# Performance work log

Hardware: AMD Instinct MI355X
Metric: run time of the kernel (lower is better)

Reference implementation:

```python
import jax, jax.numpy as jnp
import numpy as np

B, N, CIN, D, H = 4, 8192, 64, 64, 8  # batch, grid points, in_ch, per-head dim, heads
EPS = 1e-5


def layernorm(x, w, b):
    # x: [b, h, l, d]; w, b: [h, d] (per-head affine), normalize over last dim
    mu = jnp.mean(x, axis=-1, keepdims=True)
    var = jnp.var(x, axis=-1, keepdims=True)
    xn = (x - mu) * jax.lax.rsqrt(var + EPS)
    return xn * w[None, :, None, :] + b[None, :, None, :]


def setup_inputs() -> dict:
    key = jax.random.key(0)
    ks = jax.random.split(key, 12)
    hd = H * D
    s_in = 1.0 / np.sqrt(CIN)
    s_hd = 1.0 / np.sqrt(hd)
    return {
        "v": jax.random.normal(ks[0], (B, N, CIN), jnp.float32),
        "Wq_w": jax.random.uniform(ks[1], (hd, CIN), jnp.float32, -s_in, s_in),
        "Wq_b": jax.random.uniform(ks[2], (hd,), jnp.float32, -s_in, s_in),
        "Wk_w": jax.random.uniform(ks[3], (hd, CIN), jnp.float32, -s_in, s_in),
        "Wk_b": jax.random.uniform(ks[4], (hd,), jnp.float32, -s_in, s_in),
        "Wv_w": jax.random.uniform(ks[5], (hd, CIN), jnp.float32, -s_in, s_in),
        "Wv_b": jax.random.uniform(ks[6], (hd,), jnp.float32, -s_in, s_in),
        "lnq_w": jnp.ones((H, D), jnp.float32),
        "lnq_b": jnp.zeros((H, D), jnp.float32),
        "lnk_w": jnp.ones((H, D), jnp.float32),
        "lnk_b": jnp.zeros((H, D), jnp.float32),
        "o_w": jax.random.uniform(ks[7], (D, hd), jnp.float32, -s_hd, s_hd),
        "o_b": jax.random.uniform(ks[8], (D,), jnp.float32, -s_hd, s_hd),
    }


def reference(v, Wq_w, Wq_b, Wk_w, Wk_b, Wv_w, Wv_b,
              lnq_w, lnq_b, lnk_w, lnk_b, o_w, o_b):
    b, n, _ = v.shape
    # projections: [b, l, h*d] -> [b, h, l, d]
    def proj(w, bias):
        x = v @ w.T + bias
        return x.reshape(b, n, H, D).transpose(0, 2, 1, 3)
    Q = layernorm(proj(Wq_w, Wq_b), lnq_w, lnq_b)
    K = layernorm(proj(Wk_w, Wk_b), lnk_w, lnk_b)
    V = proj(Wv_w, Wv_b)
    # (Q K^T) V == Q (K^T V): no softmax, so reassociate to O(n d^2)
    KV = jnp.einsum('bhnd,bhne->bhde', K, V)      # [b, h, d, d]
    out = jnp.einsum('bhmd,bhde->bhme', Q, KV)    # [b, h, n, d]
    out = out.transpose(0, 2, 1, 3).reshape(b, n, H * D)
    out = out @ o_w.T + o_b
    return out / n
```

## Files before the change

### kernel.cpp

```cpp
#include <hip/hip_runtime.h>
#include <hip/hip_bf16.h>

#define B_   4
#define N_   8192
#define CIN_ 64
#define H_   8
#define HD_  512
#define EPS_ 1e-5f

typedef __bf16 bf16x8 __attribute__((ext_vector_type(8)));
typedef __bf16 bf16x4 __attribute__((ext_vector_type(4)));
typedef float  f32x4  __attribute__((ext_vector_type(4)));

constexpr size_t OFF_V    = 0;
constexpr size_t SZ_V     = (size_t)B_ * N_ * CIN_ * 2;
constexpr size_t OFF_WQ   = OFF_V + SZ_V;
constexpr size_t SZ_W     = (size_t)HD_ * CIN_ * 2;
constexpr size_t OFF_WK   = OFF_WQ + SZ_W;
constexpr size_t OFF_WV   = OFF_WK + SZ_W;
constexpr size_t OFF_MT   = OFF_WV + SZ_W;
constexpr size_t SZ_MT    = (size_t)B_ * 64 * HD_ * 2;
constexpr size_t OFF_PART = OFF_MT + SZ_MT;
constexpr size_t SZ_PART  = (size_t)B_ * H_ * 16 * 64 * 64 * 4;
constexpr size_t WS_NEED  = OFF_PART + SZ_PART;

template <int CTRL>
__device__ __forceinline__ float dpp_radd(float x) {
  union { float f; int i; } u, v;
  u.f = x;
  v.i = __builtin_amdgcn_update_dpp(0, u.i, CTRL, 0xF, 0xF, false);
  return x + v.f;
}
__device__ __forceinline__ float red16(float x) {
  x = dpp_radd<0x121>(x);
  x = dpp_radd<0x122>(x);
  x = dpp_radd<0x124>(x);
  x = dpp_radd<0x128>(x);
  return x;
}

__global__ __launch_bounds__(256) void prep_cast(
    const float* __restrict__ v, const float* __restrict__ wq,
    const float* __restrict__ wk, const float* __restrict__ wv,
    __bf16* __restrict__ vb, __bf16* __restrict__ wqb,
    __bf16* __restrict__ wkb, __bf16* __restrict__ wvb) {
  const int NV4 = B_ * N_ * CIN_ / 4;
  const int NW4 = HD_ * CIN_ / 4;
  int i = blockIdx.x * 256 + threadIdx.x;
  const float* src; __bf16* dst; int j;
  if (i < NV4)                { src = v;  dst = vb;  j = i; }
  else if (i < NV4 + NW4)     { src = wq; dst = wqb; j = i - NV4; }
  else if (i < NV4 + 2 * NW4) { src = wk; dst = wkb; j = i - NV4 - NW4; }
  else                        { src = wv; dst = wvb; j = i - NV4 - 2 * NW4; }
  const float4 f = reinterpret_cast<const float4*>(src)[j];
  bf16x4 o;
  o[0] = (__bf16)f.x; o[1] = (__bf16)f.y; o[2] = (__bf16)f.z; o[3] = (__bf16)f.w;
  reinterpret_cast<bf16x4*>(dst)[j] = o;
}

__global__ __launch_bounds__(256, 2) void k1_kv(
    const __bf16* __restrict__ vb, const __bf16* __restrict__ wkb,
    const __bf16* __restrict__ wvb, const float* __restrict__ kbias,
    const float* __restrict__ vbias, const float* __restrict__ lnkw,
    const float* __restrict__ lnkb, float* __restrict__ part) {
  const int ch = blockIdx.x, h = blockIdx.y, b = blockIdx.z;
  const int tid = threadIdx.x, w = tid >> 6, lane = tid & 63;
  const int l15 = lane & 15, g = lane >> 4;
  __shared__ alignas(16) char smem[73728];
  __bf16 (*Kt)[72] = reinterpret_cast<__bf16(*)[72]>(smem + w * 18432);
  __bf16 (*Vt)[72] = reinterpret_cast<__bf16(*)[72]>(smem + w * 18432 + 9216);

  const f32x4 z4 = {0.f, 0.f, 0.f, 0.f};
  f32x4 kv[4][4];
#pragma unroll
  for (int i = 0; i < 4; ++i)
#pragma unroll
    for (int j = 0; j < 4; ++j) kv[i][j] = z4;

  float kb[4], vbi[4], lw[4], lb[4];
#pragma unroll
  for (int c = 0; c < 4; ++c) {
    const int col = h * 64 + c * 16 + l15;
    kb[c] = kbias[col]; vbi[c] = vbias[col];
    lw[c] = lnkw[col];  lb[c] = lnkb[col];
  }
  bf16x8 wkf[4][2], wvf[4][2];
#pragma unroll
  for (int c = 0; c < 4; ++c)
#pragma unroll
    for (int kk = 0; kk < 2; ++kk) {
      wkf[c][kk] = *reinterpret_cast<const bf16x8*>(
          wkb + (size_t)(h * 64 + c * 16 + l15) * CIN_ + kk * 32 + g * 8);
      wvf[c][kk] = *reinterpret_cast<const bf16x8*>(
          wvb + (size_t)(h * 64 + c * 16 + l15) * CIN_ + kk * 32 + g * 8);
    }

  for (int t = 0; t < 2; ++t) {
    const int row0 = ch * 512 + w * 128 + t * 64;
    bf16x8 av[4][2];
#pragma unroll
    for (int m = 0; m < 4; ++m)
#pragma unroll
      for (int kk = 0; kk < 2; ++kk)
        av[m][kk] = *reinterpret_cast<const bf16x8*>(
            vb + ((size_t)b * N_ + row0 + m * 16 + l15) * CIN_ + kk * 32 + g * 8);

#pragma unroll
    for (int mp = 0; mp < 2; ++mp) {
      f32x4 acc[2][4];
#pragma unroll
      for (int mi = 0; mi < 2; ++mi)
#pragma unroll
        for (int c = 0; c < 4; ++c) {
          f32x4 a = z4;
          a = __builtin_amdgcn_mfma_f32_16x16x32_bf16(av[mp * 2 + mi][0], wkf[c][0], a, 0, 0, 0);
          a = __builtin_amdgcn_mfma_f32_16x16x32_bf16(av[mp * 2 + mi][1], wkf[c][1], a, 0, 0, 0);
          acc[mi][c] = a;
        }
#pragma unroll
      for (int mi = 0; mi < 2; ++mi) {
        const int m = mp * 2 + mi;
        float s[4] = {0, 0, 0, 0}, ss[4] = {0, 0, 0, 0};
#pragma unroll
        for (int c = 0; c < 4; ++c)
#pragma unroll
          for (int r = 0; r < 4; ++r) {
            float x = acc[mi][c][r] + kb[c];
            acc[mi][c][r] = x;
            s[r] += x; ss[r] += x * x;
          }
#pragma unroll
        for (int r = 0; r < 4; ++r) {
          const float S = red16(s[r]), Q = red16(ss[r]);
          const float mu = S * (1.f / 64.f);
          const float var = Q * (1.f / 64.f) - mu * mu;
          const float rstd = rsqrtf(var + EPS_);
#pragma unroll
          for (int c = 0; c < 4; ++c)
            acc[mi][c][r] = (acc[mi][c][r] - mu) * rstd * lw[c] + lb[c];
        }
#pragma unroll
        for (int c = 0; c < 4; ++c) {
          bf16x4 p;
#pragma unroll
          for (int r = 0; r < 4; ++r) p[r] = (__bf16)acc[mi][c][r];
          *reinterpret_cast<bf16x4*>(&Kt[c * 16 + l15][m * 16 + g * 4]) = p;
        }
      }
    }
#pragma unroll
    for (int mp = 0; mp < 2; ++mp) {
      f32x4 acc[2][4];
#pragma unroll
      for (int mi = 0; mi < 2; ++mi)
#pragma unroll
        for (int c = 0; c < 4; ++c) {
          f32x4 a = z4;
          a = __builtin_amdgcn_mfma_f32_16x16x32_bf16(av[mp * 2 + mi][0], wvf[c][0], a, 0, 0, 0);
          a = __builtin_amdgcn_mfma_f32_16x16x32_bf16(av[mp * 2 + mi][1], wvf[c][1], a, 0, 0, 0);
          acc[mi][c] = a;
        }
#pragma unroll
      for (int mi = 0; mi < 2; ++mi) {
        const int m = mp * 2 + mi;
#pragma unroll
        for (int c = 0; c < 4; ++c) {
          bf16x4 p;
#pragma unroll
          for (int r = 0; r < 4; ++r) p[r] = (__bf16)(acc[mi][c][r] + vbi[c]);
          *reinterpret_cast<bf16x4*>(&Vt[c * 16 + l15][m * 16 + g * 4]) = p;
        }
      }
    }

    __syncthreads();

    bf16x8 va[4][2];
#pragma unroll
    for (int et = 0; et < 4; ++et)
#pragma unroll
      for (int nk = 0; nk < 2; ++nk)
        va[et][nk] = *reinterpret_cast<const bf16x8*>(&Vt[et * 16 + l15][nk * 32 + g * 8]);
#pragma unroll
    for (int dt = 0; dt < 4; ++dt) {
      bf16x8 ka[2];
#pragma unroll
      for (int nk = 0; nk < 2; ++nk)
        ka[nk] = *reinterpret_cast<const bf16x8*>(&Kt[dt * 16 + l15][nk * 32 + g * 8]);
#pragma unroll
      for (int et = 0; et < 4; ++et) {
        kv[dt][et] = __builtin_amdgcn_mfma_f32_16x16x32_bf16(ka[0], va[et][0], kv[dt][et], 0, 0, 0);
        kv[dt][et] = __builtin_amdgcn_mfma_f32_16x16x32_bf16(ka[1], va[et][1], kv[dt][et], 0, 0, 0);
      }
    }

    __syncthreads();
  }

  float* red = reinterpret_cast<float*>(smem + w * 17408);
#pragma unroll
  for (int dt = 0; dt < 4; ++dt)
#pragma unroll
    for (int et = 0; et < 4; ++et)
      *reinterpret_cast<f32x4*>(red + (et * 16 + l15) * 68 + dt * 16 + g * 4) = kv[dt][et];
  __syncthreads();
  float* p0 = part + (size_t)((b * H_ + h) * 16 + ch) * 4096;
#pragma unroll
  for (int k = 0; k < 4; ++k) {
    const int idx4 = tid + k * 256;
    const int e = idx4 >> 4, d = (idx4 & 15) * 4;
    f32x4 sum = *reinterpret_cast<const f32x4*>(
        reinterpret_cast<const float*>(smem) + e * 68 + d);
#pragma unroll
    for (int ww = 1; ww < 4; ++ww)
      sum += *reinterpret_cast<const f32x4*>(
          reinterpret_cast<const float*>(smem + ww * 17408) + e * 68 + d);
    *reinterpret_cast<f32x4*>(p0 + idx4 * 4) = sum;
  }
}

__global__ __launch_bounds__(256) void k2_mt(const float* __restrict__ part,
                                             const float* __restrict__ ow,
                                             __bf16* __restrict__ Mt) {
  const int h = blockIdx.x, b = blockIdx.y;
  const int tid = threadIdx.x;
  __shared__ float KVt[64][64];
  __shared__ float OWl[64][64];
  const float* p0 = part + (size_t)((b * H_ + h) * 16) * 4096;
  for (int i = tid; i < 4096; i += 256) {
    float s = 0.f;
#pragma unroll
    for (int c = 0; c < 16; ++c) s += p0[(size_t)c * 4096 + i];
    (&KVt[0][0])[i] = s;
  }
  for (int i = tid; i < 4096; i += 256) {
    int E = i >> 6, c = i & 63;
    OWl[E][c] = ow[(size_t)E * HD_ + h * 64 + c];
  }
  __syncthreads();
  for (int i = tid; i < 4096; i += 256) {
    int E = i >> 6, d = i & 63;
    float s = 0.f;
#pragma unroll
    for (int c = 0; c < 64; ++c) s += KVt[c][d] * OWl[E][c];
    Mt[(size_t)(b * 64 + E) * HD_ + h * 64 + d] = (__bf16)(s * (1.0f / N_));
  }
}

__global__ __launch_bounds__(256, 2) void k3_out(
    const __bf16* __restrict__ vb, const __bf16* __restrict__ wqb,
    const float* __restrict__ qbias, const float* __restrict__ lnqw,
    const float* __restrict__ lnqb, const __bf16* __restrict__ Mt,
    const float* __restrict__ obias, float* __restrict__ out) {
  const int nt = blockIdx.x, b = blockIdx.y;
  const int tid = threadIdx.x, w = tid >> 6, lane = tid & 63;
  const int l15 = lane & 15, g = lane >> 4;
  __shared__ __bf16 Qt[64][520];
  const int row0 = nt * 64;
  const f32x4 z4 = {0.f, 0.f, 0.f, 0.f};

  bf16x8 bv[4][2];
#pragma unroll
  for (int c = 0; c < 4; ++c)
#pragma unroll
    for (int kk = 0; kk < 2; ++kk)
      bv[c][kk] = *reinterpret_cast<const bf16x8*>(
          vb + ((size_t)b * N_ + row0 + c * 16 + l15) * CIN_ + kk * 32 + g * 8);

#pragma unroll
  for (int hh = 0; hh < 2; ++hh) {
    const int h = w * 2 + hh;
    bf16x8 aw[4][2];
#pragma unroll
    for (int mj = 0; mj < 4; ++mj)
#pragma unroll
      for (int kk = 0; kk < 2; ++kk)
        aw[mj][kk] = *reinterpret_cast<const bf16x8*>(
            wqb + (size_t)(h * 64 + mj * 16 + l15) * CIN_ + kk * 32 + g * 8);
    f32x4 qb4[4], lw4[4], lb4[4];
#pragma unroll
    for (int mj = 0; mj < 4; ++mj) {
      const int base = h * 64 + mj * 16 + g * 4;
      qb4[mj] = *reinterpret_cast<const f32x4*>(qbias + base);
      lw4[mj] = *reinterpret_cast<const f32x4*>(lnqw + base);
      lb4[mj] = *reinterpret_cast<const f32x4*>(lnqb + base);
    }
    f32x4 acc[4][4];
#pragma unroll
    for (int mj = 0; mj < 4; ++mj)
#pragma unroll
      for (int c = 0; c < 4; ++c) {
        f32x4 a = z4;
        a = __builtin_amdgcn_mfma_f32_16x16x32_bf16(aw[mj][0], bv[c][0], a, 0, 0, 0);
        a = __builtin_amdgcn_mfma_f32_16x16x32_bf16(aw[mj][1], bv[c][1], a, 0, 0, 0);
        acc[mj][c] = a;
      }
#pragma unroll
    for (int c = 0; c < 4; ++c) {
      float s = 0.f, ss = 0.f;
#pragma unroll
      for (int mj = 0; mj < 4; ++mj)
#pragma unroll
        for (int r = 0; r < 4; ++r) {
          float x = acc[mj][c][r] + qb4[mj][r];
          acc[mj][c][r] = x;
          s += x; ss += x * x;
        }
      s += __shfl_xor(s, 16); ss += __shfl_xor(ss, 16);
      s += __shfl_xor(s, 32); ss += __shfl_xor(ss, 32);
      const float mu = s * (1.f / 64.f);
      const float var = ss * (1.f / 64.f) - mu * mu;
      const float rstd = rsqrtf(var + EPS_);
#pragma unroll
      for (int mj = 0; mj < 4; ++mj)
#pragma unroll
        for (int r = 0; r < 4; ++r)
          acc[mj][c][r] = (acc[mj][c][r] - mu) * rstd * lw4[mj][r] + lb4[mj][r];
    }
#pragma unroll
    for (int mj = 0; mj < 4; ++mj)
#pragma unroll
      for (int c = 0; c < 4; ++c) {
        bf16x4 p;
#pragma unroll
        for (int r = 0; r < 4; ++r) p[r] = (__bf16)acc[mj][c][r];
        *reinterpret_cast<bf16x4*>(&Qt[c * 16 + l15][h * 64 + mj * 16 + g * 4]) = p;
      }
  }
  __syncthreads();

  f32x4 acc2[4];
#pragma unroll
  for (int et = 0; et < 4; ++et) acc2[et] = z4;
  for (int kk = 0; kk < 16; ++kk) {
    bf16x8 aq = *reinterpret_cast<const bf16x8*>(&Qt[w * 16 + l15][kk * 32 + g * 8]);
#pragma unroll
    for (int et = 0; et < 4; ++et) {
      bf16x8 bm = *reinterpret_cast<const bf16x8*>(
          Mt + (size_t)(b * 64 + et * 16 + l15) * HD_ + kk * 32 + g * 8);
      acc2[et] = __builtin_amdgcn_mfma_f32_16x16x32_bf16(aq, bm, acc2[et], 0, 0, 0);
    }
  }
#pragma unroll
  for (int et = 0; et < 4; ++et) {
    const float ob = obias[et * 16 + l15] * (1.0f / N_);
#pragma unroll
    for (int r = 0; r < 4; ++r)
      out[((size_t)b * N_ + row0 + w * 16 + g * 4 + r) * 64 + et * 16 + l15] =
          acc2[et][r] + ob;
  }
}

extern "C" void kernel_launch(void* const* d_in, const int* in_sizes, int n_in,
                              void* d_out, int out_size, void* d_ws, size_t ws_size,
                              hipStream_t stream) {
  const float* v     = (const float*)d_in[0];
  const float* Wq_w  = (const float*)d_in[1];
  const float* Wq_b  = (const float*)d_in[2];
  const float* Wk_w  = (const float*)d_in[3];
  const float* Wk_b  = (const float*)d_in[4];
  const float* Wv_w  = (const float*)d_in[5];
  const float* Wv_b  = (const float*)d_in[6];
  const float* lnq_w = (const float*)d_in[7];
  const float* lnq_b = (const float*)d_in[8];
  const float* lnk_w = (const float*)d_in[9];
  const float* lnk_b = (const float*)d_in[10];
  const float* o_w   = (const float*)d_in[11];
  const float* o_b   = (const float*)d_in[12];
  float* out = (float*)d_out;
  char* ws = (char*)d_ws;
  if (ws_size < WS_NEED) return;

  __bf16* vb   = (__bf16*)(ws + OFF_V);
  __bf16* wqb  = (__bf16*)(ws + OFF_WQ);
  __bf16* wkb  = (__bf16*)(ws + OFF_WK);
  __bf16* wvb  = (__bf16*)(ws + OFF_WV);
  __bf16* Mt   = (__bf16*)(ws + OFF_MT);
  float*  part = (float*)(ws + OFF_PART);

  const int NTOT4 = B_ * N_ * CIN_ / 4 + 3 * (HD_ * CIN_ / 4);
  prep_cast<<<NTOT4 / 256, 256, 0, stream>>>(v, Wq_w, Wk_w, Wv_w, vb, wqb, wkb, wvb);
  k1_kv<<<dim3(16, H_, B_), 256, 0, stream>>>(vb, wkb, wvb, Wk_b, Wv_b, lnk_w, lnk_b, part);
  k2_mt<<<dim3(H_, B_), 256, 0, stream>>>(part, o_w, Mt);
  k3_out<<<dim3(N_ / 64, B_), 256, 0, stream>>>(vb, wqb, Wq_b, lnq_w, lnq_b, Mt, o_b, out);
}
```

Before: 70.91 us.

## Split KV reduction into more chunks, parallelize M build, hoist M fragments in output

```diff
diff --git a/kernel.cpp b/kernel.cpp
--- a/kernel.cpp
+++ b/kernel.cpp
@@ -7,6 +7,7 @@
 #define H_   8
 #define HD_  512
 #define EPS_ 1e-5f
+#define NCH_ 32
 
 typedef __bf16 bf16x8 __attribute__((ext_vector_type(8)));
 typedef __bf16 bf16x4 __attribute__((ext_vector_type(4)));
@@ -19,9 +20,11 @@
 constexpr size_t OFF_WK   = OFF_WQ + SZ_W;
 constexpr size_t OFF_WV   = OFF_WK + SZ_W;
 constexpr size_t OFF_MT   = OFF_WV + SZ_W;
-constexpr size_t SZ_MT    = (size_t)B_ * 64 * HD_ * 2;
-constexpr size_t OFF_PART = OFF_MT + SZ_MT;
-constexpr size_t SZ_PART  = (size_t)B_ * H_ * 16 * 64 * 64 * 4;
+constexpr size_t SZ_MT    = (size_t)B_ * 64 * HD_ * 4;
+constexpr size_t OFF_KVG  = OFF_MT + SZ_MT;
+constexpr size_t SZ_KVG   = (size_t)B_ * H_ * 4096 * 4;
+constexpr size_t OFF_PART = OFF_KVG + SZ_KVG;
+constexpr size_t SZ_PART  = (size_t)B_ * H_ * NCH_ * 4096 * 4;
 constexpr size_t WS_NEED  = OFF_PART + SZ_PART;
 
 template <int CTRL>
@@ -95,107 +98,105 @@
           wvb + (size_t)(h * 64 + c * 16 + l15) * CIN_ + kk * 32 + g * 8);
     }
 
-  for (int t = 0; t < 2; ++t) {
-    const int row0 = ch * 512 + w * 128 + t * 64;
-    bf16x8 av[4][2];
-#pragma unroll
-    for (int m = 0; m < 4; ++m)
-#pragma unroll
-      for (int kk = 0; kk < 2; ++kk)
-        av[m][kk] = *reinterpret_cast<const bf16x8*>(
-            vb + ((size_t)b * N_ + row0 + m * 16 + l15) * CIN_ + kk * 32 + g * 8);
-
-#pragma unroll
-    for (int mp = 0; mp < 2; ++mp) {
-      f32x4 acc[2][4];
-#pragma unroll
-      for (int mi = 0; mi < 2; ++mi)
-#pragma unroll
-        for (int c = 0; c < 4; ++c) {
-          f32x4 a = z4;
-          a = __builtin_amdgcn_mfma_f32_16x16x32_bf16(av[mp * 2 + mi][0], wkf[c][0], a, 0, 0, 0);
-          a = __builtin_amdgcn_mfma_f32_16x16x32_bf16(av[mp * 2 + mi][1], wkf[c][1], a, 0, 0, 0);
-          acc[mi][c] = a;
+  const int row0 = ch * 256 + w * 64;
+  bf16x8 av[4][2];
+#pragma unroll
+  for (int m = 0; m < 4; ++m)
+#pragma unroll
+    for (int kk = 0; kk < 2; ++kk)
+      av[m][kk] = *reinterpret_cast<const bf16x8*>(
+          vb + ((size_t)b * N_ + row0 + m * 16 + l15) * CIN_ + kk * 32 + g * 8);
+
+#pragma unroll
+  for (int mp = 0; mp < 2; ++mp) {
+    f32x4 acc[2][4];
+#pragma unroll
+    for (int mi = 0; mi < 2; ++mi)
+#pragma unroll
+      for (int c = 0; c < 4; ++c) {
+        f32x4 a = z4;
+        a = __builtin_amdgcn_mfma_f32_16x16x32_bf16(av[mp * 2 + mi][0], wkf[c][0], a, 0, 0, 0);
+        a = __builtin_amdgcn_mfma_f32_16x16x32_bf16(av[mp * 2 + mi][1], wkf[c][1], a, 0, 0, 0);
+        acc[mi][c] = a;
+      }
+#pragma unroll
+    for (int mi = 0; mi < 2; ++mi) {
+      const int m = mp * 2 + mi;
+      float s[4] = {0, 0, 0, 0}, ss[4] = {0, 0, 0, 0};
+#pragma unroll
+      for (int c = 0; c < 4; ++c)
+#pragma unroll
+        for (int r = 0; r < 4; ++r) {
+          float x = acc[mi][c][r] + kb[c];
+          acc[mi][c][r] = x;
+          s[r] += x; ss[r] += x * x;
         }
 #pragma unroll
-      for (int mi = 0; mi < 2; ++mi) {
-        const int m = mp * 2 + mi;
-        float s[4] = {0, 0, 0, 0}, ss[4] = {0, 0, 0, 0};
+      for (int r = 0; r < 4; ++r) {
+        const float S = red16(s[r]), Q = red16(ss[r]);
+        const float mu = S * (1.f / 64.f);
+        const float var = Q * (1.f / 64.f) - mu * mu;
+        const float rstd = rsqrtf(var + EPS_);
 #pragma unroll
         for (int c = 0; c < 4; ++c)
-#pragma unroll
-          for (int r = 0; r < 4; ++r) {
-            float x = acc[mi][c][r] + kb[c];
-            acc[mi][c][r] = x;
-            s[r] += x; ss[r] += x * x;
-          }
-#pragma unroll
-        for (int r = 0; r < 4; ++r) {
-          const float S = red16(s[r]), Q = red16(ss[r]);
-          const float mu = S * (1.f / 64.f);
-          const float var = Q * (1.f / 64.f) - mu * mu;
-          const float rstd = rsqrtf(var + EPS_);
-#pragma unroll
-          for (int c = 0; c < 4; ++c)
-            acc[mi][c][r] = (acc[mi][c][r] - mu) * rstd * lw[c] + lb[c];
-        }
-#pragma unroll
-        for (int c = 0; c < 4; ++c) {
-          bf16x4 p;
-#pragma unroll
-          for (int r = 0; r < 4; ++r) p[r] = (__bf16)acc[mi][c][r];
-          *reinterpret_cast<bf16x4*>(&Kt[c * 16 + l15][m * 16 + g * 4]) = p;
-        }
-      }
-    }
-#pragma unroll
-    for (int mp = 0; mp < 2; ++mp) {
-      f32x4 acc[2][4];
-#pragma unroll
-      for (int mi = 0; mi < 2; ++mi)
-#pragma unroll
-        for (int c = 0; c < 4; ++c) {
-          f32x4 a = z4;
-          a = __builtin_amdgcn_mfma_f32_16x16x32_bf16(av[mp * 2 + mi][0], wvf[c][0], a, 0, 0, 0);
-          a = __builtin_amdgcn_mfma_f32_16x16x32_bf16(av[mp * 2 + mi][1], wvf[c][1], a, 0, 0, 0);
-          acc[mi][c] = a;
-        }
-#pragma unroll
-      for (int mi = 0; mi < 2; ++mi) {
-        const int m = mp * 2 + mi;
-#pragma unroll
-        for (int c = 0; c < 4; ++c) {
-          bf16x4 p;
-#pragma unroll
-          for (int r = 0; r < 4; ++r) p[r] = (__bf16)(acc[mi][c][r] + vbi[c]);
-          *reinterpret_cast<bf16x4*>(&Vt[c * 16 + l15][m * 16 + g * 4]) = p;
-        }
-      }
-    }
-
-    __syncthreads();
-
-    bf16x8 va[4][2];
-#pragma unroll
-    for (int et = 0; et < 4; ++et)
-#pragma unroll
-      for (int nk = 0; nk < 2; ++nk)
-        va[et][nk] = *reinterpret_cast<const bf16x8*>(&Vt[et * 16 + l15][nk * 32 + g * 8]);
-#pragma unroll
-    for (int dt = 0; dt < 4; ++dt) {
-      bf16x8 ka[2];
-#pragma unroll
-      for (int nk = 0; nk < 2; ++nk)
-        ka[nk] = *reinterpret_cast<const bf16x8*>(&Kt[dt * 16 + l15][nk * 32 + g * 8]);
-#pragma unroll
-      for (int et = 0; et < 4; ++et) {
-        kv[dt][et] = __builtin_amdgcn_mfma_f32_16x16x32_bf16(ka[0], va[et][0], kv[dt][et], 0, 0, 0);
-        kv[dt][et] = __builtin_amdgcn_mfma_f32_16x16x32_bf16(ka[1], va[et][1], kv[dt][et], 0, 0, 0);
-      }
-    }
-
-    __syncthreads();
-  }
+          acc[mi][c][r] = (acc[mi][c][r] - mu) * rstd * lw[c] + lb[c];
+      }
+#pragma unroll
+      for (int c = 0; c < 4; ++c) {
+        bf16x4 p;
+#pragma unroll
+        for (int r = 0; r < 4; ++r) p[r] = (__bf16)acc[mi][c][r];
+        *reinterpret_cast<bf16x4*>(&Kt[c * 16 + l15][m * 16 + g * 4]) = p;
+      }
+    }
+  }
+#pragma unroll
+  for (int mp = 0; mp < 2; ++mp) {
+    f32x4 acc[2][4];
+#pragma unroll
+    for (int mi = 0; mi < 2; ++mi)
+#pragma unroll
+      for (int c = 0; c < 4; ++c) {
+        f32x4 a = z4;
+        a = __builtin_amdgcn_mfma_f32_16x16x32_bf16(av[mp * 2 + mi][0], wvf[c][0], a, 0, 0, 0);
+        a = __builtin_amdgcn_mfma_f32_16x16x32_bf16(av[mp * 2 + mi][1], wvf[c][1], a, 0, 0, 0);
+        acc[mi][c] = a;
+      }
+#pragma unroll
+    for (int mi = 0; mi < 2; ++mi) {
+      const int m = mp * 2 + mi;
+#pragma unroll
+      for (int c = 0; c < 4; ++c) {
+        bf16x4 p;
+#pragma unroll
+        for (int r = 0; r < 4; ++r) p[r] = (__bf16)(acc[mi][c][r] + vbi[c]);
+        *reinterpret_cast<bf16x4*>(&Vt[c * 16 + l15][m * 16 + g * 4]) = p;
+      }
+    }
+  }
+
+  __syncthreads();
+
+  bf16x8 va[4][2];
+#pragma unroll
+  for (int et = 0; et < 4; ++et)
+#pragma unroll
+    for (int nk = 0; nk < 2; ++nk)
+      va[et][nk] = *reinterpret_cast<const bf16x8*>(&Vt[et * 16 + l15][nk * 32 + g * 8]);
+#pragma unroll
+  for (int dt = 0; dt < 4; ++dt) {
+    bf16x8 ka[2];
+#pragma unroll
+    for (int nk = 0; nk < 2; ++nk)
+      ka[nk] = *reinterpret_cast<const bf16x8*>(&Kt[dt * 16 + l15][nk * 32 + g * 8]);
+#pragma unroll
+    for (int et = 0; et < 4; ++et) {
+      kv[dt][et] = __builtin_amdgcn_mfma_f32_16x16x32_bf16(ka[0], va[et][0], kv[dt][et], 0, 0, 0);
+      kv[dt][et] = __builtin_amdgcn_mfma_f32_16x16x32_bf16(ka[1], va[et][1], kv[dt][et], 0, 0, 0);
+    }
+  }
+
+  __syncthreads();
 
   float* red = reinterpret_cast<float*>(smem + w * 17408);
 #pragma unroll
@@ -204,7 +205,7 @@
     for (int et = 0; et < 4; ++et)
       *reinterpret_cast<f32x4*>(red + (et * 16 + l15) * 68 + dt * 16 + g * 4) = kv[dt][et];
   __syncthreads();
-  float* p0 = part + (size_t)((b * H_ + h) * 16 + ch) * 4096;
+  float* p0 = part + (size_t)((b * H_ + h) * NCH_ + ch) * 4096;
 #pragma unroll
   for (int k = 0; k < 4; ++k) {
     const int idx4 = tid + k * 256;
@@ -219,38 +220,44 @@
   }
 }
 
-__global__ __launch_bounds__(256) void k2_mt(const float* __restrict__ part,
-                                             const float* __restrict__ ow,
-                                             __bf16* __restrict__ Mt) {
-  const int h = blockIdx.x, b = blockIdx.y;
+__global__ __launch_bounds__(256) void k2a_reduce(const float* __restrict__ part,
+                                                 float* __restrict__ KVg) {
+  const int s = blockIdx.x, h = blockIdx.y, b = blockIdx.z;
+  const int idx = s * 256 + threadIdx.x;
+  const float* p0 = part + (size_t)((b * H_ + h) * NCH_) * 4096 + idx;
+  float acc = 0.f;
+#pragma unroll 8
+  for (int ch = 0; ch < NCH_; ++ch) acc += p0[(size_t)ch * 4096];
+  KVg[(size_t)(b * H_ + h) * 4096 + idx] = acc;
+}
+
+__global__ __launch_bounds__(256) void k2b_mt(const float* __restrict__ KVg,
+                                              const float* __restrict__ ow,
+                                              float* __restrict__ Mt) {
+  const int z = blockIdx.x, h = blockIdx.y, b = blockIdx.z;
   const int tid = threadIdx.x;
-  __shared__ float KVt[64][64];
-  __shared__ float OWl[64][64];
-  const float* p0 = part + (size_t)((b * H_ + h) * 16) * 4096;
-  for (int i = tid; i < 4096; i += 256) {
-    float s = 0.f;
-#pragma unroll
-    for (int c = 0; c < 16; ++c) s += p0[(size_t)c * 4096 + i];
-    (&KVt[0][0])[i] = s;
-  }
-  for (int i = tid; i < 4096; i += 256) {
+  __shared__ float KVl[4096];
+  __shared__ float OWl[16][65];
+  const float* kv0 = KVg + (size_t)(b * H_ + h) * 4096;
+  for (int i = tid; i < 4096; i += 256) KVl[i] = kv0[i];
+  for (int i = tid; i < 16 * 64; i += 256) {
     int E = i >> 6, c = i & 63;
-    OWl[E][c] = ow[(size_t)E * HD_ + h * 64 + c];
+    OWl[E][c] = ow[(size_t)(z * 16 + E) * HD_ + h * 64 + c];
   }
   __syncthreads();
-  for (int i = tid; i < 4096; i += 256) {
+  for (int i = tid; i < 1024; i += 256) {
     int E = i >> 6, d = i & 63;
     float s = 0.f;
 #pragma unroll
-    for (int c = 0; c < 64; ++c) s += KVt[c][d] * OWl[E][c];
-    Mt[(size_t)(b * 64 + E) * HD_ + h * 64 + d] = (__bf16)(s * (1.0f / N_));
+    for (int c = 0; c < 64; ++c) s += KVl[c * 64 + d] * OWl[E][c];
+    Mt[(size_t)(b * 64 + z * 16 + E) * HD_ + h * 64 + d] = s * (1.0f / N_);
   }
 }
 
 __global__ __launch_bounds__(256, 2) void k3_out(
     const __bf16* __restrict__ vb, const __bf16* __restrict__ wqb,
     const float* __restrict__ qbias, const float* __restrict__ lnqw,
-    const float* __restrict__ lnqb, const __bf16* __restrict__ Mt,
+    const float* __restrict__ lnqb, const float* __restrict__ MtF,
     const float* __restrict__ obias, float* __restrict__ out) {
   const int nt = blockIdx.x, b = blockIdx.y;
   const int tid = threadIdx.x, w = tid >> 6, lane = tid & 63;
@@ -327,27 +334,44 @@
         *reinterpret_cast<bf16x4*>(&Qt[c * 16 + l15][h * 64 + mj * 16 + g * 4]) = p;
       }
   }
+
+  bf16x8 mhi[16], mlo[16];
+  {
+    const float* mrow = MtF + ((size_t)b * 64 + w * 16 + l15) * HD_ + g * 8;
+#pragma unroll
+    for (int kk = 0; kk < 16; ++kk) {
+      const f32x4 x0 = *reinterpret_cast<const f32x4*>(mrow + kk * 32);
+      const f32x4 x1 = *reinterpret_cast<const f32x4*>(mrow + kk * 32 + 4);
+      bf16x8 hi, lo;
+#pragma unroll
+      for (int r = 0; r < 4; ++r) {
+        hi[r] = (__bf16)x0[r];     lo[r] = (__bf16)(x0[r] - (float)hi[r]);
+        hi[4 + r] = (__bf16)x1[r]; lo[4 + r] = (__bf16)(x1[r] - (float)hi[4 + r]);
+      }
+      mhi[kk] = hi; mlo[kk] = lo;
+    }
+  }
   __syncthreads();
 
   f32x4 acc2[4];
 #pragma unroll
   for (int et = 0; et < 4; ++et) acc2[et] = z4;
   for (int kk = 0; kk < 16; ++kk) {
-    bf16x8 aq = *reinterpret_cast<const bf16x8*>(&Qt[w * 16 + l15][kk * 32 + g * 8]);
 #pragma unroll
     for (int et = 0; et < 4; ++et) {
-      bf16x8 bm = *reinterpret_cast<const bf16x8*>(
-          Mt + (size_t)(b * 64 + et * 16 + l15) * HD_ + kk * 32 + g * 8);
-      acc2[et] = __builtin_amdgcn_mfma_f32_16x16x32_bf16(aq, bm, acc2[et], 0, 0, 0);
-    }
-  }
+      bf16x8 bq = *reinterpret_cast<const bf16x8*>(&Qt[et * 16 + l15][kk * 32 + g * 8]);
+      acc2[et] = __builtin_amdgcn_mfma_f32_16x16x32_bf16(mhi[kk], bq, acc2[et], 0, 0, 0);
+      acc2[et] = __builtin_amdgcn_mfma_f32_16x16x32_bf16(mlo[kk], bq, acc2[et], 0, 0, 0);
+    }
+  }
+  f32x4 ob4;
+#pragma unroll
+  for (int r = 0; r < 4; ++r) ob4[r] = obias[w * 16 + g * 4 + r] * (1.0f / N_);
 #pragma unroll
   for (int et = 0; et < 4; ++et) {
-    const float ob = obias[et * 16 + l15] * (1.0f / N_);
-#pragma unroll
-    for (int r = 0; r < 4; ++r)
-      out[((size_t)b * N_ + row0 + w * 16 + g * 4 + r) * 64 + et * 16 + l15] =
-          acc2[et][r] + ob;
+    f32x4 res = acc2[et] + ob4;
+    *reinterpret_cast<f32x4*>(
+        out + ((size_t)b * N_ + row0 + et * 16 + l15) * 64 + w * 16 + g * 4) = res;
   }
 }
 
@@ -375,12 +399,14 @@
   __bf16* wqb  = (__bf16*)(ws + OFF_WQ);
   __bf16* wkb  = (__bf16*)(ws + OFF_WK);
   __bf16* wvb  = (__bf16*)(ws + OFF_WV);
-  __bf16* Mt   = (__bf16*)(ws + OFF_MT);
+  float*  Mt   = (float*)(ws + OFF_MT);
+  float*  KVg  = (float*)(ws + OFF_KVG);
   float*  part = (float*)(ws + OFF_PART);
 
   const int NTOT4 = B_ * N_ * CIN_ / 4 + 3 * (HD_ * CIN_ / 4);
   prep_cast<<<NTOT4 / 256, 256, 0, stream>>>(v, Wq_w, Wk_w, Wv_w, vb, wqb, wkb, wvb);
-  k1_kv<<<dim3(16, H_, B_), 256, 0, stream>>>(vb, wkb, wvb, Wk_b, Wv_b, lnk_w, lnk_b, part);
-  k2_mt<<<dim3(H_, B_), 256, 0, stream>>>(part, o_w, Mt);
+  k1_kv<<<dim3(NCH_, H_, B_), 256, 0, stream>>>(vb, wkb, wvb, Wk_b, Wv_b, lnk_w, lnk_b, part);
+  k2a_reduce<<<dim3(16, H_, B_), 256, 0, stream>>>(part, KVg);
+  k2b_mt<<<dim3(4, H_, B_), 256, 0, stream>>>(KVg, o_w, Mt);
   k3_out<<<dim3(N_ / 64, B_), 256, 0, stream>>>(vb, wqb, Wq_b, lnq_w, lnq_b, Mt, o_b, out);
 }
```

New measurement: 61.26 us. -13.6%, faster.
